# Kernel optimization log

Measured on AMD Instinct MI355X. Metric: run time of the kernel, lower is better.

## Reference

```python
import jax, jax.numpy as jnp
import numpy as np

B, S, D, H, HD, FF, V = 256, 512, 128, 4, 32, 512, 256
THRESHOLD = 4.0


def _ln(x, g, b, eps=1e-5):
    m = x.mean(-1, keepdims=True)
    v = jnp.var(x, axis=-1, keepdims=True)  # biased var, matches torch LayerNorm
    return (x - m) / jnp.sqrt(v + eps) * g + b


def setup_inputs() -> dict:
    key = jax.random.key(0)
    ks = jax.random.split(key, 10)
    g = lambda i, shape: jax.random.normal(ks[i], shape, jnp.float32) * 0.05
    return {
        "input_bytes": jax.random.randint(ks[0], (B, S), 0, V, jnp.int32),
        "emb": g(1, (V, D)),
        "pos_emb": g(2, (S, D)),
        "ln_g": jnp.ones((D,), jnp.float32), "ln_b": jnp.zeros((D,), jnp.float32),
        "attn_w": g(3, (2, 3 * D, D)), "attn_b": jnp.zeros((2, 3 * D), jnp.float32),
        "out_w": g(4, (2, D, D)), "out_b": jnp.zeros((2, D), jnp.float32),
        "ff1_w": g(5, (2, FF, D)), "ff1_b": jnp.zeros((2, FF), jnp.float32),
        "ff2_w": g(6, (2, D, FF)), "ff2_b": jnp.zeros((2, D), jnp.float32),
        "n1_g": jnp.ones((2, D), jnp.float32), "n1_b": jnp.zeros((2, D), jnp.float32),
        "n2_g": jnp.ones((2, D), jnp.float32), "n2_b": jnp.zeros((2, D), jnp.float32),
        "proj_w": g(7, (V, D)), "proj_b": jnp.zeros((V,), jnp.float32),
    }


def _avg_entropy(input_bytes, emb, pos_emb, ln_g, ln_b, attn_w, attn_b, out_w,
                 out_b, ff1_w, ff1_b, ff2_w, ff2_b, n1_g, n1_b, n2_g, n2_b,
                 proj_w, proj_b):
    h = emb[input_bytes] + pos_emb[None, :, :]          # [B,S,D]
    h = _ln(h, ln_g, ln_b)
    scale = jnp.asarray(1.0 / np.sqrt(HD), jnp.float32)
    for l in range(2):  # post-norm TransformerEncoderLayer, relu FFN
        qkv = h @ attn_w[l].T + attn_b[l]               # [B,S,3D]
        q, k, v = jnp.split(qkv, 3, axis=-1)
        q = q.reshape(B, S, H, HD)
        k = k.reshape(B, S, H, HD)
        v = v.reshape(B, S, H, HD)
        scores = jnp.einsum('bqhd,bkhd->bhqk', q, k) * scale
        a = jax.nn.softmax(scores, axis=-1)
        o = jnp.einsum('bhqk,bkhd->bqhd', a, v).reshape(B, S, D)
        o = o @ out_w[l].T + out_b[l]
        h = _ln(h + o, n1_g[l], n1_b[l])
        f = jax.nn.relu(h @ ff1_w[l].T + ff1_b[l]) @ ff2_w[l].T + ff2_b[l]
        h = _ln(h + f, n2_g[l], n2_b[l])
    logits = h @ proj_w.T + proj_b                      # [B,S,256]
    probs = jax.nn.softmax(logits, axis=-1)
    entropy = -jnp.sum(probs * jnp.log(probs + 1e-10), axis=-1)  # [B,S]
    return entropy.mean(axis=0)                         # [S]


def reference(input_bytes, emb, pos_emb, ln_g, ln_b, attn_w, attn_b, out_w,
              out_b, ff1_w, ff1_b, ff2_w, ff2_b, n1_g, n1_b, n2_g, n2_b,
              proj_w, proj_b):
    avg_entropy = _avg_entropy(input_bytes, emb, pos_emb, ln_g, ln_b, attn_w,
                               attn_b, out_w, out_b, ff1_w, ff1_b, ff2_w,
                               ff2_b, n1_g, n1_b, n2_g, n2_b, proj_w, proj_b)
    # Fixed-shape form of the entropy-threshold patch segmentation:
    # boundary[i]=1 iff a new patch starts at i (i>=1 and avg_entropy[i]>thr).
    boundary = jnp.concatenate([
        jnp.zeros((1,), jnp.int32),
        (avg_entropy[1:] > THRESHOLD).astype(jnp.int32),
    ])
    segment_ids = jnp.cumsum(boundary)                  # patch id per position
    return avg_entropy, segment_ids
```

## Files before the change

kernel.cpp:

```cpp
#include <hip/hip_runtime.h>


#define AS1 __attribute__((address_space(1)))
#define AS3 __attribute__((address_space(3)))

typedef __bf16 bf16x8 __attribute__((ext_vector_type(8)));
typedef float  f32x4  __attribute__((ext_vector_type(4)));

__device__ __forceinline__ unsigned short f2bf(float f) {
  union { float f; unsigned int u; } c; c.f = f;
  unsigned int u = c.u;
  u += 0x7FFFu + ((u >> 16) & 1u);
  return (unsigned short)(u >> 16);
}
__device__ __forceinline__ float bf2f(unsigned short u) {
  union { unsigned int u; float f; } c; c.u = ((unsigned int)u) << 16;
  return c.f;
}

__device__ __forceinline__ float EXP2(float x) {
#if __has_builtin(__builtin_amdgcn_exp2f)
  return __builtin_amdgcn_exp2f(x);
#else
  return exp2f(x);
#endif
}

__device__ __forceinline__ void async_copy16(const void* g, void* l) {
  __builtin_amdgcn_global_load_lds((AS1 void*)(void*)g, (AS3 void*)l, 16, 0, 0);
}

__device__ __forceinline__ unsigned int cvtpk_bf16(float lo, float hi) {
  unsigned int r;
  asm("v_cvt_pk_bf16_f32 %0, %1, %2" : "=v"(r) : "v"(lo), "v"(hi));
  return r;
}
__device__ __forceinline__ void plswap32(unsigned int& a, unsigned int& b) {
  asm("v_permlane32_swap_b32 %0, %1" : "+v"(a), "+v"(b));
}
__device__ __forceinline__ void plswap16(unsigned int& a, unsigned int& b) {
  asm("v_permlane16_swap_b32 %0, %1" : "+v"(a), "+v"(b));
}

#define MFMA __builtin_amdgcn_mfma_f32_16x16x32_bf16

__global__ void conv_permA(const float* __restrict__ src,
                           unsigned short* __restrict__ dst, int K, int n) {
  int i = blockIdx.x * 256 + threadIdx.x;
  if (i >= n) return;
  int row = i / K, k = i - row * K;
  int frag = (row >> 4) * (K >> 5) + (k >> 5);
  int d = frag * 512 + ((k >> 3) & 3) * 128 + (row & 15) * 8 + (k & 7);
  dst[d] = f2bf(src[i]);
}

#define QSCALE 0.2550602989892646f
__global__ void conv_attn_w(const float* __restrict__ src,
                            unsigned short* __restrict__ dst) {
  int i = blockIdx.x * 256 + threadIdx.x;
  int r = (i >> 7) % 384;
  float v = src[i];
  if (r < 128) v *= QSCALE;
  dst[i] = f2bf(v);
}
__global__ void conv_attn_b(const float* __restrict__ src,
                            float* __restrict__ dst) {
  int i = blockIdx.x * 256 + threadIdx.x;
  if (i < 768) {
    float v = src[i];
    if ((i % 384) < 128) v *= QSCALE;
    dst[i] = v;
  }
}

__global__ __launch_bounds__(256) void embed_ln(
    const int* __restrict__ bytes, const float* __restrict__ emb,
    const float* __restrict__ pos, const float* __restrict__ g,
    const float* __restrict__ bta, unsigned short* __restrict__ hbf) {
  int wv = threadIdx.x >> 6, lane = threadIdx.x & 63;
  int tok = blockIdx.x * 4 + wv;
  int s = tok & 511;
  int bidx = bytes[tok];
  const float* e = emb + (size_t)bidx * 128;
  const float* p = pos + (size_t)s * 128;
  float x0 = e[lane] + p[lane];
  float x1 = e[lane + 64] + p[lane + 64];
  float sum = x0 + x1, ssq = x0 * x0 + x1 * x1;
#pragma unroll
  for (int off = 32; off; off >>= 1) {
    sum += __shfl_xor(sum, off);
    ssq += __shfl_xor(ssq, off);
  }
  float mean = sum * 0.0078125f;
  float var = ssq * 0.0078125f - mean * mean;
  float rs = rsqrtf(var + 1e-5f);
  float y0 = (x0 - mean) * rs * g[lane] + bta[lane];
  float y1 = (x1 - mean) * rs * g[lane + 64] + bta[lane + 64];
  size_t o = (size_t)tok * 128;
  hbf[o + lane] = f2bf(y0); hbf[o + lane + 64] = f2bf(y1);
}

__global__ __launch_bounds__(256) void gemm_qkv(
    const unsigned short* __restrict__ A, const unsigned short* __restrict__ W,
    const float* __restrict__ bias, unsigned short* __restrict__ Cout,
    int M, int N, int K) {
  __shared__ __bf16 As[128 * 64];
  __shared__ __bf16 Ws[128 * 64];
  const int t = threadIdx.x;
  const int lane = t & 63, w = t >> 6;
  const int m0 = blockIdx.y * 128, n0 = blockIdx.x * 128;
  const int wm = (w >> 1) * 64, wn = (w & 1) * 64;
  f32x4 acc[4][4] = {};
  const int srow = w * 32 + (lane >> 3);
  const int scol = (lane & 7) * 8;

  for (int k0 = 0; k0 < K; k0 += 64) {
#pragma unroll
    for (int j = 0; j < 4; ++j) {
      int r = srow + j * 8;
      int ldsrow = w * 32 + j * 8;
      async_copy16(A + (size_t)(m0 + r) * K + k0 + scol, &As[ldsrow * 64]);
      async_copy16(W + (size_t)(n0 + r) * K + k0 + scol, &Ws[ldsrow * 64]);
    }
    __syncthreads();
#pragma unroll
    for (int kk = 0; kk < 2; ++kk) {
      bf16x8 af[4], bfr[4];
#pragma unroll
      for (int f = 0; f < 4; ++f) {
        af[f]  = *(const bf16x8*)&As[(wm + f * 16 + (lane & 15)) * 64 + kk * 32 + (lane >> 4) * 8];
        bfr[f] = *(const bf16x8*)&Ws[(wn + f * 16 + (lane & 15)) * 64 + kk * 32 + (lane >> 4) * 8];
      }
#pragma unroll
      for (int fi = 0; fi < 4; ++fi)
#pragma unroll
        for (int fj = 0; fj < 4; ++fj)
          acc[fi][fj] = MFMA(af[fi], bfr[fj], acc[fi][fj], 0, 0, 0);
    }
    __syncthreads();
  }

#pragma unroll
  for (int fj = 0; fj < 4; ++fj) {
    int col = n0 + wn + fj * 16 + (lane & 15);
    float bv = bias[col];
#pragma unroll
    for (int fi = 0; fi < 4; ++fi) {
#pragma unroll
      for (int r2 = 0; r2 < 4; ++r2) {
        int row = m0 + wm + fi * 16 + (lane >> 4) * 4 + r2;
        Cout[(size_t)row * N + col] = f2bf(acc[fi][fj][r2] + bv);
      }
    }
  }
}

__global__ __launch_bounds__(256) void oproj_ln(
    const unsigned short* __restrict__ A, const unsigned short* __restrict__ Wp,
    const float* __restrict__ bias, unsigned short* __restrict__ h,
    const float* __restrict__ gamma, const float* __restrict__ beta) {
  const int lane = threadIdx.x & 63, w = threadIdx.x >> 6;
  const int c = lane & 15, g = lane >> 4;
  const size_t tok0 = (size_t)blockIdx.x * 128 + w * 32;

  bf16x8 at[2][4];
#pragma unroll
  for (int tf = 0; tf < 2; ++tf)
#pragma unroll
    for (int kk = 0; kk < 4; ++kk)
      at[tf][kk] =
          *(const bf16x8*)(A + (tok0 + tf * 16 + c) * 128 + kk * 32 + g * 8);

  f32x4 acc[8][2] = {};
#pragma unroll
  for (int db = 0; db < 8; ++db)
#pragma unroll
    for (int kk = 0; kk < 4; ++kk) {
      bf16x8 wf = *(const bf16x8*)(Wp + (db * 4 + kk) * 512 + lane * 8);
      acc[db][0] = MFMA(wf, at[0][kk], acc[db][0], 0, 0, 0);
      acc[db][1] = MFMA(wf, at[1][kk], acc[db][1], 0, 0, 0);
    }

#pragma unroll
  for (int tf = 0; tf < 2; ++tf) {
    unsigned short* hrow = h + (tok0 + tf * 16 + c) * 128;
    float x[8][4];
    float s_ = 0.f, q_ = 0.f;
#pragma unroll
    for (int db = 0; db < 8; ++db) {
      float4 bv = *(const float4*)(bias + db * 16 + g * 4);
      ushort4 rv = *(const ushort4*)(hrow + db * 16 + g * 4);
      x[db][0] = acc[db][tf][0] + bv.x + bf2f(rv.x);
      x[db][1] = acc[db][tf][1] + bv.y + bf2f(rv.y);
      x[db][2] = acc[db][tf][2] + bv.z + bf2f(rv.z);
      x[db][3] = acc[db][tf][3] + bv.w + bf2f(rv.w);
#pragma unroll
      for (int r = 0; r < 4; ++r) { s_ += x[db][r]; q_ += x[db][r] * x[db][r]; }
    }
    s_ += __shfl_xor(s_, 16); s_ += __shfl_xor(s_, 32);
    q_ += __shfl_xor(q_, 16); q_ += __shfl_xor(q_, 32);
    float mean = s_ * 0.0078125f;
    float var = q_ * 0.0078125f - mean * mean;
    float rs = rsqrtf(var + 1e-5f);
#pragma unroll
    for (int db = 0; db < 8; ++db) {
      float4 gv = *(const float4*)(gamma + db * 16 + g * 4);
      float4 bb = *(const float4*)(beta + db * 16 + g * 4);
      ushort4 o;
      o.x = f2bf((x[db][0] - mean) * rs * gv.x + bb.x);
      o.y = f2bf((x[db][1] - mean) * rs * gv.y + bb.y);
      o.z = f2bf((x[db][2] - mean) * rs * gv.z + bb.z);
      o.w = f2bf((x[db][3] - mean) * rs * gv.w + bb.w);
      *(ushort4*)(hrow + db * 16 + g * 4) = o;
    }
  }
}

__global__ __launch_bounds__(256) void ffn_reg(
    unsigned short* __restrict__ h, const unsigned short* __restrict__ W1p,
    const float* __restrict__ b1, const unsigned short* __restrict__ W2p,
    const float* __restrict__ b2, const float* __restrict__ gamma,
    const float* __restrict__ beta) {
  const int lane = threadIdx.x & 63, w = threadIdx.x >> 6;
  const int c = lane & 15, g = lane >> 4;
  const size_t tok0 = (size_t)blockIdx.x * 128 + w * 32;

  bf16x8 at[2][4];
#pragma unroll
  for (int tf = 0; tf < 2; ++tf)
#pragma unroll
    for (int kk = 0; kk < 4; ++kk)
      at[tf][kk] =
          *(const bf16x8*)(h + (tok0 + tf * 16 + c) * 128 + kk * 32 + g * 8);

  f32x4 acc[8][2] = {};
  for (int s = 0; s < 16; ++s) {
    f32x4 d1[2][2] = {};
#pragma unroll
    for (int kk = 0; kk < 4; ++kk) {
      bf16x8 wa = *(const bf16x8*)(W1p + ((2 * s) * 4 + kk) * 512 + lane * 8);
      bf16x8 wb = *(const bf16x8*)(W1p + ((2 * s + 1) * 4 + kk) * 512 + lane * 8);
      d1[0][0] = MFMA(wa, at[0][kk], d1[0][0], 0, 0, 0);
      d1[0][1] = MFMA(wa, at[1][kk], d1[0][1], 0, 0, 0);
      d1[1][0] = MFMA(wb, at[0][kk], d1[1][0], 0, 0, 0);
      d1[1][1] = MFMA(wb, at[1][kk], d1[1][1], 0, 0, 0);
    }
    float4 bva = *(const float4*)(b1 + s * 32 + g * 4);
    float4 bvb = *(const float4*)(b1 + s * 32 + 16 + g * 4);
    bf16x8 gp[2];
#pragma unroll
    for (int tf = 0; tf < 2; ++tf) {
      float pa0 = fmaxf(d1[0][tf][0] + bva.x, 0.f);
      float pa1 = fmaxf(d1[0][tf][1] + bva.y, 0.f);
      float pa2 = fmaxf(d1[0][tf][2] + bva.z, 0.f);
      float pa3 = fmaxf(d1[0][tf][3] + bva.w, 0.f);
      float pb0 = fmaxf(d1[1][tf][0] + bvb.x, 0.f);
      float pb1 = fmaxf(d1[1][tf][1] + bvb.y, 0.f);
      float pb2 = fmaxf(d1[1][tf][2] + bvb.z, 0.f);
      float pb3 = fmaxf(d1[1][tf][3] + bvb.w, 0.f);
      unsigned int w00 = cvtpk_bf16(pa0, pa1), w01 = cvtpk_bf16(pa2, pa3);
      unsigned int w10 = cvtpk_bf16(pb0, pb1), w11 = cvtpk_bf16(pb2, pb3);
      plswap32(w00, w10); plswap16(w00, w10);
      plswap32(w01, w11); plswap16(w01, w11);
      union { unsigned int u[4]; bf16x8 v; } pk;
      pk.u[0] = w00; pk.u[1] = w01; pk.u[2] = w10; pk.u[3] = w11;
      gp[tf] = pk.v;
    }
#pragma unroll
    for (int db = 0; db < 8; ++db) {
      bf16x8 w2 = *(const bf16x8*)(W2p + (db * 16 + s) * 512 + lane * 8);
      acc[db][0] = MFMA(w2, gp[0], acc[db][0], 0, 0, 0);
      acc[db][1] = MFMA(w2, gp[1], acc[db][1], 0, 0, 0);
    }
  }

#pragma unroll
  for (int tf = 0; tf < 2; ++tf) {
    unsigned short* hrow = h + (tok0 + tf * 16 + c) * 128;
    float x[8][4];
    float s_ = 0.f, q_ = 0.f;
#pragma unroll
    for (int db = 0; db < 8; ++db) {
      float4 bv = *(const float4*)(b2 + db * 16 + g * 4);
      ushort4 rv = *(const ushort4*)(hrow + db * 16 + g * 4);
      x[db][0] = acc[db][tf][0] + bv.x + bf2f(rv.x);
      x[db][1] = acc[db][tf][1] + bv.y + bf2f(rv.y);
      x[db][2] = acc[db][tf][2] + bv.z + bf2f(rv.z);
      x[db][3] = acc[db][tf][3] + bv.w + bf2f(rv.w);
#pragma unroll
      for (int r = 0; r < 4; ++r) { s_ += x[db][r]; q_ += x[db][r] * x[db][r]; }
    }
    s_ += __shfl_xor(s_, 16); s_ += __shfl_xor(s_, 32);
    q_ += __shfl_xor(q_, 16); q_ += __shfl_xor(q_, 32);
    float mean = s_ * 0.0078125f;
    float var = q_ * 0.0078125f - mean * mean;
    float rs = rsqrtf(var + 1e-5f);
#pragma unroll
    for (int db = 0; db < 8; ++db) {
      float4 gv = *(const float4*)(gamma + db * 16 + g * 4);
      float4 bb = *(const float4*)(beta + db * 16 + g * 4);
      ushort4 o;
      o.x = f2bf((x[db][0] - mean) * rs * gv.x + bb.x);
      o.y = f2bf((x[db][1] - mean) * rs * gv.y + bb.y);
      o.z = f2bf((x[db][2] - mean) * rs * gv.z + bb.z);
      o.w = f2bf((x[db][3] - mean) * rs * gv.w + bb.w);
      *(ushort4*)(hrow + db * 16 + g * 4) = o;
    }
  }
}

__global__ __launch_bounds__(256) void vocab_entropy(
    const unsigned short* __restrict__ h, const unsigned short* __restrict__ Wp,
    const float* __restrict__ bias, float* __restrict__ ent) {
  const int lane = threadIdx.x & 63, w = threadIdx.x >> 6;
  const int c = lane & 15, g = lane >> 4;
  const size_t tok0 = (size_t)blockIdx.x * 128 + w * 32;

  bf16x8 at[2][4];
#pragma unroll
  for (int tf = 0; tf < 2; ++tf)
#pragma unroll
    for (int kk = 0; kk < 4; ++kk)
      at[tf][kk] =
          *(const bf16x8*)(h + (tok0 + tf * 16 + c) * 128 + kk * 32 + g * 8);

  f32x4 acc[16][2] = {};
#pragma unroll
  for (int vb = 0; vb < 16; ++vb)
#pragma unroll
    for (int kk = 0; kk < 4; ++kk) {
      bf16x8 wf = *(const bf16x8*)(Wp + (vb * 4 + kk) * 512 + lane * 8);
      acc[vb][0] = MFMA(wf, at[0][kk], acc[vb][0], 0, 0, 0);
      acc[vb][1] = MFMA(wf, at[1][kk], acc[vb][1], 0, 0, 0);
    }

  const float L2E = 1.4426950408889634f;
#pragma unroll
  for (int tf = 0; tf < 2; ++tf) {
    float m_ = -1e30f;
#pragma unroll
    for (int vb = 0; vb < 16; ++vb) {
      float4 bv = *(const float4*)(bias + vb * 16 + g * 4);
      acc[vb][tf][0] += bv.x; acc[vb][tf][1] += bv.y;
      acc[vb][tf][2] += bv.z; acc[vb][tf][3] += bv.w;
      m_ = fmaxf(m_, fmaxf(fmaxf(acc[vb][tf][0], acc[vb][tf][1]),
                           fmaxf(acc[vb][tf][2], acc[vb][tf][3])));
    }
    m_ = fmaxf(m_, __shfl_xor(m_, 16));
    m_ = fmaxf(m_, __shfl_xor(m_, 32));
    float z_ = 0.f, sx_ = 0.f;
#pragma unroll
    for (int vb = 0; vb < 16; ++vb)
#pragma unroll
      for (int r = 0; r < 4; ++r) {
        float xx = acc[vb][tf][r];
        float e = EXP2((xx - m_) * L2E);
        z_ += e; sx_ += e * xx;
      }
    z_ += __shfl_xor(z_, 16);  z_ += __shfl_xor(z_, 32);
    sx_ += __shfl_xor(sx_, 16); sx_ += __shfl_xor(sx_, 32);
    if (g == 0) ent[tok0 + tf * 16 + c] = m_ + logf(z_) - sx_ / z_;
  }
}

__global__ __launch_bounds__(512, 4) void attn_mfma(
    const unsigned short* __restrict__ qkv, unsigned short* __restrict__ obf) {
  __shared__ __bf16 Ks[512 * 40];
  __shared__ __bf16 Vt[32 * 520];

  const int hh = blockIdx.x & 3, bl = blockIdx.x >> 2;
  const int t = threadIdx.x;
  const int lane = t & 63, wv = t >> 6;
  const int c = lane & 15, g = lane >> 4;
  const size_t tok0 = (size_t)bl * 512;

  {
    const unsigned short* kr = qkv + (tok0 + t) * 384 + 128 + hh * 32;
    bf16x8 k0 = *(const bf16x8*)(kr);
    bf16x8 k1 = *(const bf16x8*)(kr + 8);
    bf16x8 k2 = *(const bf16x8*)(kr + 16);
    bf16x8 k3 = *(const bf16x8*)(kr + 24);
    __bf16* kd = Ks + t * 40;
    *(bf16x8*)(kd + 0) = k0;  *(bf16x8*)(kd + 8) = k1;
    *(bf16x8*)(kd + 16) = k2; *(bf16x8*)(kd + 24) = k3;
    const unsigned short* vr = kr + 128;
    bf16x8 v0 = *(const bf16x8*)(vr);
    bf16x8 v1 = *(const bf16x8*)(vr + 8);
    bf16x8 v2 = *(const bf16x8*)(vr + 16);
    bf16x8 v3 = *(const bf16x8*)(vr + 24);
#pragma unroll
    for (int i = 0; i < 8; ++i) {
      Vt[(i)      * 520 + t] = v0[i];
      Vt[(i + 8)  * 520 + t] = v1[i];
      Vt[(i + 16) * 520 + t] = v2[i];
      Vt[(i + 24) * 520 + t] = v3[i];
    }
  }

  bf16x8 qb[4];
  {
    const unsigned short* qp = qkv + (tok0 + wv * 64) * 384 + hh * 32;
#pragma unroll
    for (int qf = 0; qf < 4; ++qf)
      qb[qf] = *(const bf16x8*)(qp + (size_t)(qf * 16 + c) * 384 + g * 8);
  }
  __syncthreads();

  f32x4 ot[4][2] = {};
  float l[4] = {0.f, 0.f, 0.f, 0.f};
  const f32x4 zz = {0.f, 0.f, 0.f, 0.f};

  for (int kt = 0; kt < 8; ++kt) {
    bf16x8 ka[4];
#pragma unroll
    for (int kf = 0; kf < 4; ++kf)
      ka[kf] = *(const bf16x8*)&Ks[(kt * 64 + kf * 16 + c) * 40 + g * 8];
    bf16x8 vb[2][2];
#pragma unroll
    for (int hf = 0; hf < 2; ++hf)
#pragma unroll
      for (int ksl = 0; ksl < 2; ++ksl)
        vb[hf][ksl] =
            *(const bf16x8*)&Vt[(hf * 16 + c) * 520 + kt * 64 + ksl * 32 + g * 8];

#pragma unroll
    for (int qf = 0; qf < 4; ++qf) {
      f32x4 sA = MFMA(ka[0], qb[qf], zz, 0, 0, 0);
      f32x4 sB = MFMA(ka[1], qb[qf], zz, 0, 0, 0);
      f32x4 sC = MFMA(ka[2], qb[qf], zz, 0, 0, 0);
      f32x4 sD = MFMA(ka[3], qb[qf], zz, 0, 0, 0);

      {
        float pa0 = EXP2(sA[0]), pa1 = EXP2(sA[1]);
        float pa2 = EXP2(sA[2]), pa3 = EXP2(sA[3]);
        float pb0 = EXP2(sB[0]), pb1 = EXP2(sB[1]);
        float pb2 = EXP2(sB[2]), pb3 = EXP2(sB[3]);
        l[qf] += ((pa0 + pa1) + (pa2 + pa3)) + ((pb0 + pb1) + (pb2 + pb3));
        unsigned int w00 = cvtpk_bf16(pa0, pa1), w01 = cvtpk_bf16(pa2, pa3);
        unsigned int w10 = cvtpk_bf16(pb0, pb1), w11 = cvtpk_bf16(pb2, pb3);
        plswap32(w00, w10); plswap16(w00, w10);
        plswap32(w01, w11); plswap16(w01, w11);
        union { unsigned int u[4]; bf16x8 v; } pk;
        pk.u[0] = w00; pk.u[1] = w01; pk.u[2] = w10; pk.u[3] = w11;
        ot[qf][0] = MFMA(vb[0][0], pk.v, ot[qf][0], 0, 0, 0);
        ot[qf][1] = MFMA(vb[1][0], pk.v, ot[qf][1], 0, 0, 0);
      }
      {
        float pa0 = EXP2(sC[0]), pa1 = EXP2(sC[1]);
        float pa2 = EXP2(sC[2]), pa3 = EXP2(sC[3]);
        float pb0 = EXP2(sD[0]), pb1 = EXP2(sD[1]);
        float pb2 = EXP2(sD[2]), pb3 = EXP2(sD[3]);
        l[qf] += ((pa0 + pa1) + (pa2 + pa3)) + ((pb0 + pb1) + (pb2 + pb3));
        unsigned int w00 = cvtpk_bf16(pa0, pa1), w01 = cvtpk_bf16(pa2, pa3);
        unsigned int w10 = cvtpk_bf16(pb0, pb1), w11 = cvtpk_bf16(pb2, pb3);
        plswap32(w00, w10); plswap16(w00, w10);
        plswap32(w01, w11); plswap16(w01, w11);
        union { unsigned int u[4]; bf16x8 v; } pk;
        pk.u[0] = w00; pk.u[1] = w01; pk.u[2] = w10; pk.u[3] = w11;
        ot[qf][0] = MFMA(vb[0][1], pk.v, ot[qf][0], 0, 0, 0);
        ot[qf][1] = MFMA(vb[1][1], pk.v, ot[qf][1], 0, 0, 0);
      }
    }
  }

#pragma unroll
  for (int qf = 0; qf < 4; ++qf) {
    l[qf] += __shfl_xor(l[qf], 16);
    l[qf] += __shfl_xor(l[qf], 32);
  }
#pragma unroll
  for (int qf = 0; qf < 4; ++qf) {
    float rl = 1.0f / l[qf];
#pragma unroll
    for (int hf = 0; hf < 2; ++hf) {
      ushort4 pk;
      pk.x = f2bf(ot[qf][hf][0] * rl);
      pk.y = f2bf(ot[qf][hf][1] * rl);
      pk.z = f2bf(ot[qf][hf][2] * rl);
      pk.w = f2bf(ot[qf][hf][3] * rl);
      *(ushort4*)(obf + (tok0 + wv * 64 + qf * 16 + c) * 128 + hh * 32 +
                  hf * 16 + g * 4) = pk;
    }
  }
}

__global__ __launch_bounds__(64) void avg_entropy_kernel(
    const float* __restrict__ ent, float* __restrict__ out) {
  int s = blockIdx.x, lane = threadIdx.x;
  float a = 0.f;
  for (int b = lane; b < 256; b += 64) a += ent[(size_t)b * 512 + s];
#pragma unroll
  for (int off = 32; off; off >>= 1) a += __shfl_xor(a, off);
  if (lane == 0) out[s] = a * 0.00390625f;
}

__global__ __launch_bounds__(512) void seg_kernel(float* out) {
  __shared__ int cs[512];
  int i = threadIdx.x;
  float e = out[i];
  cs[i] = (i >= 1 && e > 4.0f) ? 1 : 0;
  __syncthreads();
  for (int off = 1; off < 512; off <<= 1) {
    int v = (i >= off) ? cs[i - off] : 0;
    __syncthreads();
    cs[i] += v;
    __syncthreads();
  }
  out[512 + i] = (float)cs[i];
}

extern "C" void kernel_launch(void* const* d_in, const int* in_sizes, int n_in,
                              void* d_out, int out_size, void* d_ws,
                              size_t ws_size, hipStream_t stream) {
  (void)in_sizes; (void)n_in; (void)out_size; (void)ws_size;
  const int*   input_bytes = (const int*)d_in[0];
  const float* emb    = (const float*)d_in[1];
  const float* pos    = (const float*)d_in[2];
  const float* ln_g   = (const float*)d_in[3];
  const float* ln_b   = (const float*)d_in[4];
  const float* attn_w = (const float*)d_in[5];
  const float* attn_b = (const float*)d_in[6];
  const float* out_w  = (const float*)d_in[7];
  const float* out_b  = (const float*)d_in[8];
  const float* ff1_w  = (const float*)d_in[9];
  const float* ff1_b  = (const float*)d_in[10];
  const float* ff2_w  = (const float*)d_in[11];
  const float* ff2_b  = (const float*)d_in[12];
  const float* n1_g   = (const float*)d_in[13];
  const float* n1_b   = (const float*)d_in[14];
  const float* n2_g   = (const float*)d_in[15];
  const float* n2_b   = (const float*)d_in[16];
  const float* proj_w = (const float*)d_in[17];
  const float* proj_b = (const float*)d_in[18];

  char* ws = (char*)d_ws;
  unsigned short* hbf  = (unsigned short*)(ws);
  unsigned short* obf  = (unsigned short*)(ws + 33554432);
  unsigned short* qkvc = (unsigned short*)(ws + 67108864);
  unsigned short* wbf  = (unsigned short*)(ws + 167772160);
  float*          absb = (float*)(ws + 168624128);
  float*          entb = (float*)(ws + 168628224);

  unsigned short* attnw_bf = wbf;
  unsigned short* outwA    = wbf + 98304;
  unsigned short* w1A      = wbf + 131072;
  unsigned short* w2A      = wbf + 262144;
  unsigned short* projA    = wbf + 393216;

  conv_attn_w<<<384, 256, 0, stream>>>(attn_w, attnw_bf);
  conv_attn_b<<<3, 256, 0, stream>>>(attn_b, absb);
  for (int l = 0; l < 2; ++l) {
    conv_permA<<<64, 256, 0, stream>>>(out_w + l * 16384, outwA + l * 16384,
                                       128, 16384);
    conv_permA<<<256, 256, 0, stream>>>(ff1_w + l * 65536, w1A + l * 65536,
                                        128, 65536);
    conv_permA<<<256, 256, 0, stream>>>(ff2_w + l * 65536, w2A + l * 65536,
                                        512, 65536);
  }
  conv_permA<<<128, 256, 0, stream>>>(proj_w, projA, 128, 32768);

  embed_ln<<<32768, 256, 0, stream>>>(input_bytes, emb, pos, ln_g, ln_b, hbf);

  for (int l = 0; l < 2; ++l) {
    gemm_qkv<<<dim3(3, 1024), 256, 0, stream>>>(
        hbf, attnw_bf + l * 49152, absb + l * 384, qkvc, 131072, 384, 128);
    attn_mfma<<<1024, 512, 0, stream>>>(qkvc, obf);
    oproj_ln<<<1024, 256, 0, stream>>>(obf, outwA + l * 16384, out_b + l * 128,
                                       hbf, n1_g + l * 128, n1_b + l * 128);
    ffn_reg<<<1024, 256, 0, stream>>>(hbf, w1A + l * 65536, ff1_b + l * 512,
                                      w2A + l * 65536, ff2_b + l * 128,
                                      n2_g + l * 128, n2_b + l * 128);
  }

  vocab_entropy<<<1024, 256, 0, stream>>>(hbf, projA, proj_b, entb);
  avg_entropy_kernel<<<512, 64, 0, stream>>>(entb, (float*)d_out);
  seg_kernel<<<1, 512, 0, stream>>>((float*)d_out);
}
```

Before: 500.0 us.

## Replace LDS-tiled QKV GEMM with register-resident activation kernel using pre-permuted weights

Swaps the generic LDS-staged QKV GEMM for a kernel that loads each warp's 32-token activation tile into registers once and streams pre-permuted weight fragments directly from global memory into MFMA. The attention weight conversion now writes an MFMA-fragment layout so each lane's fragment is a single 16-byte load. This removes the LDS staging, the barriers, and the 3x re-read of activations across N tiles. The cost is that weights are re-read from global/L2 by every warp, and the bias is fetched as vector loads with packed output stores.

```diff
diff --git a/kernel.cpp b/kernel.cpp
--- a/kernel.cpp
+++ b/kernel.cpp
@@ -24,10 +24,6 @@
 #else
   return exp2f(x);
 #endif
-}
-
-__device__ __forceinline__ void async_copy16(const void* g, void* l) {
-  __builtin_amdgcn_global_load_lds((AS1 void*)(void*)g, (AS3 void*)l, 16, 0, 0);
 }
 
 __device__ __forceinline__ unsigned int cvtpk_bf16(float lo, float hi) {
@@ -55,13 +51,16 @@
 }
 
 #define QSCALE 0.2550602989892646f
-__global__ void conv_attn_w(const float* __restrict__ src,
-                            unsigned short* __restrict__ dst) {
+__global__ void conv_attn_wA(const float* __restrict__ src,
+                             unsigned short* __restrict__ dst) {
   int i = blockIdx.x * 256 + threadIdx.x;
-  int r = (i >> 7) % 384;
+  int l = i / 49152, rem = i - l * 49152;
+  int row = rem >> 7, k = rem & 127;
   float v = src[i];
-  if (r < 128) v *= QSCALE;
-  dst[i] = f2bf(v);
+  if (row < 128) v *= QSCALE;
+  int frag = (row >> 4) * 4 + (k >> 5);
+  int d = frag * 512 + ((k >> 3) & 3) * 128 + (row & 15) * 8 + (k & 7);
+  dst[l * 49152 + d] = f2bf(v);
 }
 __global__ void conv_attn_b(const float* __restrict__ src,
                             float* __restrict__ dst) {
@@ -100,56 +99,44 @@
   hbf[o + lane] = f2bf(y0); hbf[o + lane + 64] = f2bf(y1);
 }
 
-__global__ __launch_bounds__(256) void gemm_qkv(
-    const unsigned short* __restrict__ A, const unsigned short* __restrict__ W,
-    const float* __restrict__ bias, unsigned short* __restrict__ Cout,
-    int M, int N, int K) {
-  __shared__ __bf16 As[128 * 64];
-  __shared__ __bf16 Ws[128 * 64];
-  const int t = threadIdx.x;
-  const int lane = t & 63, w = t >> 6;
-  const int m0 = blockIdx.y * 128, n0 = blockIdx.x * 128;
-  const int wm = (w >> 1) * 64, wn = (w & 1) * 64;
-  f32x4 acc[4][4] = {};
-  const int srow = w * 32 + (lane >> 3);
-  const int scol = (lane & 7) * 8;
-
-  for (int k0 = 0; k0 < K; k0 += 64) {
-#pragma unroll
-    for (int j = 0; j < 4; ++j) {
-      int r = srow + j * 8;
-      int ldsrow = w * 32 + j * 8;
-      async_copy16(A + (size_t)(m0 + r) * K + k0 + scol, &As[ldsrow * 64]);
-      async_copy16(W + (size_t)(n0 + r) * K + k0 + scol, &Ws[ldsrow * 64]);
-    }
-    __syncthreads();
-#pragma unroll
-    for (int kk = 0; kk < 2; ++kk) {
-      bf16x8 af[4], bfr[4];
-#pragma unroll
-      for (int f = 0; f < 4; ++f) {
-        af[f]  = *(const bf16x8*)&As[(wm + f * 16 + (lane & 15)) * 64 + kk * 32 + (lane >> 4) * 8];
-        bfr[f] = *(const bf16x8*)&Ws[(wn + f * 16 + (lane & 15)) * 64 + kk * 32 + (lane >> 4) * 8];
+__global__ __launch_bounds__(256) void qkv_reg(
+    const unsigned short* __restrict__ h, const unsigned short* __restrict__ Wp,
+    const float* __restrict__ bias, unsigned short* __restrict__ qkv) {
+  const int lane = threadIdx.x & 63, w = threadIdx.x >> 6;
+  const int c = lane & 15, g = lane >> 4;
+  const size_t tok0 = (size_t)blockIdx.x * 128 + w * 32;
+
+  bf16x8 at[2][4];
+#pragma unroll
+  for (int tf = 0; tf < 2; ++tf)
+#pragma unroll
+    for (int kk = 0; kk < 4; ++kk)
+      at[tf][kk] =
+          *(const bf16x8*)(h + (tok0 + tf * 16 + c) * 128 + kk * 32 + g * 8);
+
+  for (int seg = 0; seg < 3; ++seg) {
+    f32x4 acc[8][2] = {};
+#pragma unroll
+    for (int db = 0; db < 8; ++db)
+#pragma unroll
+      for (int kk = 0; kk < 4; ++kk) {
+        bf16x8 wf =
+            *(const bf16x8*)(Wp + ((seg * 8 + db) * 4 + kk) * 512 + lane * 8);
+        acc[db][0] = MFMA(wf, at[0][kk], acc[db][0], 0, 0, 0);
+        acc[db][1] = MFMA(wf, at[1][kk], acc[db][1], 0, 0, 0);
       }
 #pragma unroll
-      for (int fi = 0; fi < 4; ++fi)
-#pragma unroll
-        for (int fj = 0; fj < 4; ++fj)
-          acc[fi][fj] = MFMA(af[fi], bfr[fj], acc[fi][fj], 0, 0, 0);
-    }
-    __syncthreads();
-  }
-
-#pragma unroll
-  for (int fj = 0; fj < 4; ++fj) {
-    int col = n0 + wn + fj * 16 + (lane & 15);
-    float bv = bias[col];
-#pragma unroll
-    for (int fi = 0; fi < 4; ++fi) {
-#pragma unroll
-      for (int r2 = 0; r2 < 4; ++r2) {
-        int row = m0 + wm + fi * 16 + (lane >> 4) * 4 + r2;
-        Cout[(size_t)row * N + col] = f2bf(acc[fi][fj][r2] + bv);
+    for (int tf = 0; tf < 2; ++tf) {
+      unsigned short* orow = qkv + (tok0 + tf * 16 + c) * 384 + seg * 128;
+#pragma unroll
+      for (int db = 0; db < 8; ++db) {
+        float4 bv = *(const float4*)(bias + seg * 128 + db * 16 + g * 4);
+        ushort4 o;
+        o.x = f2bf(acc[db][tf][0] + bv.x);
+        o.y = f2bf(acc[db][tf][1] + bv.y);
+        o.z = f2bf(acc[db][tf][2] + bv.z);
+        o.w = f2bf(acc[db][tf][3] + bv.w);
+        *(ushort4*)(orow + db * 16 + g * 4) = o;
       }
     }
   }
@@ -541,13 +528,13 @@
   float*          absb = (float*)(ws + 168624128);
   float*          entb = (float*)(ws + 168628224);
 
-  unsigned short* attnw_bf = wbf;
-  unsigned short* outwA    = wbf + 98304;
-  unsigned short* w1A      = wbf + 131072;
-  unsigned short* w2A      = wbf + 262144;
-  unsigned short* projA    = wbf + 393216;
-
-  conv_attn_w<<<384, 256, 0, stream>>>(attn_w, attnw_bf);
+  unsigned short* attnwA = wbf;
+  unsigned short* outwA  = wbf + 98304;
+  unsigned short* w1A    = wbf + 131072;
+  unsigned short* w2A    = wbf + 262144;
+  unsigned short* projA  = wbf + 393216;
+
+  conv_attn_wA<<<384, 256, 0, stream>>>(attn_w, attnwA);
   conv_attn_b<<<3, 256, 0, stream>>>(attn_b, absb);
   for (int l = 0; l < 2; ++l) {
     conv_permA<<<64, 256, 0, stream>>>(out_w + l * 16384, outwA + l * 16384,
@@ -562,8 +549,8 @@
   embed_ln<<<32768, 256, 0, stream>>>(input_bytes, emb, pos, ln_g, ln_b, hbf);
 
   for (int l = 0; l < 2; ++l) {
-    gemm_qkv<<<dim3(3, 1024), 256, 0, stream>>>(
-        hbf, attnw_bf + l * 49152, absb + l * 384, qkvc, 131072, 384, 128);
+    qkv_reg<<<1024, 256, 0, stream>>>(hbf, attnwA + l * 49152, absb + l * 384,
+                                      qkvc);
     attn_mfma<<<1024, 512, 0, stream>>>(qkvc, obf);
     oproj_ln<<<1024, 256, 0, stream>>>(obf, outwA + l * 16384, out_b + l * 128,
                                        hbf, n1_g + l * 128, n1_b + l * 128);
```

New measurement: 571.6 us. 14.3% more time.
